# Kernel tuning notes

Measured on AMD Instinct MI355X. Metric: run time of the kernel, lower is better.

Reference implementation:

```python
import jax, jax.numpy as jnp
import numpy as np

NUM_EXPERTS = 8
K = 2
N_EMBD = 1024
HIDDEN = 4 * N_EMBD
BATCH = 2
SEQ = 1024
LB_SCALE = 0.01
NOISY_STD = 1.0
INIT_S = 0.02


def setup_inputs() -> dict:
    key = jax.random.key(0)
    ks = jax.random.split(key, 8)
    D, H, E = N_EMBD, HIDDEN, NUM_EXPERTS
    return {
        "x": jax.random.normal(ks[0], (BATCH, SEQ, D), jnp.float32),
        "noise": jax.random.normal(ks[1], (BATCH, SEQ, E), jnp.float32),  # torch.randn_like(logits)
        "gate_w": jax.random.normal(ks[2], (E, D), jnp.float32) * INIT_S,
        "noise_weight": jnp.zeros((E,), jnp.float32),  # initialized to zeros in the module
        "w1": jax.random.normal(ks[3], (E, H, D), jnp.float32) * INIT_S,
        "b1": jnp.zeros((E, H), jnp.float32),
        "w2": jax.random.normal(ks[4], (E, H, D), jnp.float32) * INIT_S,
        "b2": jnp.zeros((E, H), jnp.float32),
        "wp": jax.random.normal(ks[5], (E, D, H), jnp.float32) * INIT_S,
        "bp": jnp.zeros((E, D), jnp.float32),
    }


def reference(x, noise, gate_w, noise_weight, w1, b1, w2, b2, wp, bp):
    B, S, D = x.shape
    E = gate_w.shape[0]

    # ---- TopKGateParallel ----
    logits = jnp.einsum('bsd,ed->bse', x, gate_w)           # [B,S,E]
    gate_weights = jax.nn.softmax(logits, axis=-1)
    gw_mean = gate_weights.reshape(-1, E).mean(axis=0)       # [E]
    load_balance_loss = jnp.mean((gw_mean - 1.0 / E) ** 2) * LB_SCALE  # mse vs uniform

    logits_noisy = logits + (noise * NOISY_STD) * noise_weight
    top_v, top_i = jax.lax.top_k(logits_noisy, K)            # [B,S,K]
    # scatter top-k logits into a -inf sea, then softmax -> zeros at non-topk slots
    topk_mask = jnp.sum(jax.nn.one_hot(top_i, E, dtype=jnp.float32), axis=-2) > 0  # [B,S,E]
    sparse_logits = jnp.where(topk_mask, logits_noisy, -jnp.inf)
    top_k_gated_weights = jax.nn.softmax(sparse_logits, axis=-1)  # [B,S,E]

    # ---- expert compute + weighted combine (world_size=1: all experts local) ----
    x_flat = x.reshape(B * S, D)                              # [T,D]
    w_flat = top_k_gated_weights.reshape(B * S, E)            # [T,E]
    y = jnp.zeros_like(x_flat)
    for e in range(E):  # fixed small set of experts
        h = x_flat @ w1[e].T + b1[e]                          # [T,H]
        g = x_flat @ w2[e].T + b2[e]                          # [T,H]
        out_e = (h * jax.nn.silu(g)) @ wp[e].T + bp[e]        # [T,D]
        y = y + w_flat[:, e:e + 1] * out_e
    y = y.reshape(B, S, D)
    return y, load_balance_loss
```

## Files before the change

### kernel.cpp

```cpp
#include <hip/hip_runtime.h>

#define TOK 2048
#define DIM 1024
#define HID 4096
#define NE 8
#define KSPLIT 4
#define TMAX 24
#define NCAST 2048

typedef unsigned short u16;
typedef __attribute__((ext_vector_type(8))) short s16x8;
typedef __attribute__((ext_vector_type(4))) float f32x4;

__device__ __forceinline__ u16 f2b(float f) {
  unsigned u = __builtin_bit_cast(unsigned, f);
  unsigned r = (u + 0x7fffu + ((u >> 16) & 1u)) >> 16;
  return (u16)r;
}

__device__ __forceinline__ void gld_lds16(const void* g, void* l) {
  __builtin_amdgcn_global_load_lds((const __attribute__((address_space(1))) void*)g,
                                   (__attribute__((address_space(3))) void*)l, 16, 0, 0);
}

__global__ __launch_bounds__(256) void k_gate(const float* __restrict__ x,
    const float* __restrict__ noise, const float* __restrict__ gw,
    const float* __restrict__ nw, const float* __restrict__ w1,
    const float* __restrict__ w2, const float* __restrict__ wp,
    u16* __restrict__ w1b, u16* __restrict__ w2b, u16* __restrict__ wpb,
    int* __restrict__ tok_e, float* __restrict__ tok_w,
    int* __restrict__ bhist, float* __restrict__ bgw, u16* __restrict__ x16) {
  if (blockIdx.x >= TOK / 4) {
    const int cb = blockIdx.x - TOK / 4;
    const size_t NPT = (size_t)NE * HID * DIM;
    const size_t stride = (size_t)NCAST * 256 * 8;
    for (size_t i = ((size_t)cb * 256 + threadIdx.x) * 8; i < 3 * NPT; i += stride) {
      const float* in; u16* o; size_t j;
      if (i < NPT)          { in = w1; o = w1b; j = i; }
      else if (i < 2 * NPT) { in = w2; o = w2b; j = i - NPT; }
      else                  { in = wp; o = wpb; j = i - 2 * NPT; }
      float4 a = *(const float4*)(in + j);
      float4 b = *(const float4*)(in + j + 4);
      u16 u[8];
      u[0] = f2b(a.x); u[1] = f2b(a.y); u[2] = f2b(a.z); u[3] = f2b(a.w);
      u[4] = f2b(b.x); u[5] = f2b(b.y); u[6] = f2b(b.z); u[7] = f2b(b.w);
      *(s16x8*)(o + j) = *(const s16x8*)u;
    }
    return;
  }
  const int wid = threadIdx.x >> 6, lane = threadIdx.x & 63;
  const int t = blockIdx.x * 4 + wid;
  const float* xr = x + (size_t)t * DIM + lane * 16;
  float acc[NE];
#pragma unroll
  for (int e = 0; e < NE; ++e) acc[e] = 0.f;
  u16 xb[16];
#pragma unroll
  for (int j = 0; j < 4; ++j) {
    float4 xv = *(const float4*)(xr + j * 4);
    xb[j * 4 + 0] = f2b(xv.x); xb[j * 4 + 1] = f2b(xv.y);
    xb[j * 4 + 2] = f2b(xv.z); xb[j * 4 + 3] = f2b(xv.w);
#pragma unroll
    for (int e = 0; e < NE; ++e) {
      float4 gv = *(const float4*)(gw + e * DIM + lane * 16 + j * 4);
      acc[e] += xv.x * gv.x + xv.y * gv.y + xv.z * gv.z + xv.w * gv.w;
    }
  }
  *(s16x8*)(x16 + (size_t)t * DIM + lane * 16) = *(const s16x8*)xb;
  *(s16x8*)(x16 + (size_t)t * DIM + lane * 16 + 8) = *(const s16x8*)(xb + 8);
#pragma unroll
  for (int e = 0; e < NE; ++e) {
#pragma unroll
    for (int off = 32; off >= 1; off >>= 1) acc[e] += __shfl_xor(acc[e], off);
  }
  float m = acc[0];
#pragma unroll
  for (int e = 1; e < NE; ++e) m = fmaxf(m, acc[e]);
  float p[NE]; float s = 0.f;
#pragma unroll
  for (int e = 0; e < NE; ++e) { p[e] = expf(acc[e] - m); s += p[e]; }
  float inv = 1.f / s;
  float v[NE];
#pragma unroll
  for (int e = 0; e < NE; ++e) v[e] = acc[e] + noise[t * NE + e] * nw[e];
  float v0 = -3.4e38f, v1 = -3.4e38f; int i0 = 0, i1 = 0;
#pragma unroll
  for (int e = 0; e < NE; ++e) {
    float ve = v[e];
    if (ve > v0) { v1 = v0; i1 = i0; v0 = ve; i0 = e; }
    else if (ve > v1) { v1 = ve; i1 = e; }
  }
  float e1 = expf(v1 - v0);
  float den = 1.f + e1;
  float w0 = 1.f / den, w1v = e1 / den;

  __shared__ float pl[4][NE];
  __shared__ int el[4][2];
  if (lane == 0) {
#pragma unroll
    for (int e = 0; e < NE; ++e) pl[wid][e] = p[e] * inv;
    el[wid][0] = i0; el[wid][1] = i1;
    tok_e[t * 2] = i0; tok_e[t * 2 + 1] = i1;
    tok_w[t * 2] = w0; tok_w[t * 2 + 1] = w1v;
  }
  __syncthreads();
  if (threadIdx.x < NE) {
    const int e = threadIdx.x;
    float ps = pl[0][e] + pl[1][e] + pl[2][e] + pl[3][e];
    int h = 0;
#pragma unroll
    for (int j = 0; j < 4; ++j) {
      h += (el[j][0] == e);
      h += (el[j][1] == e);
    }
    bgw[blockIdx.x * NE + e] = ps;
    bhist[blockIdx.x * NE + e] = h;
  }
}

__global__ __launch_bounds__(512) void k_scan(const int* __restrict__ bhist,
    const float* __restrict__ bgw, int* __restrict__ blk_off, int* __restrict__ prefix,
    int* __restrict__ counts, int* __restrict__ tile_tab, float* __restrict__ loss_out) {
  const int i = threadIdx.x, lane = i & 63, wv = i >> 6;
  __shared__ int wsum[8];
  __shared__ float wfs[8];
  __shared__ int etot[8];
  __shared__ float fsum[8];
  for (int e = 0; e < NE; ++e) {
    int v = bhist[i * NE + e];
    int sc = v;
#pragma unroll
    for (int off = 1; off < 64; off <<= 1) {
      int u = __shfl_up(sc, off);
      if (lane >= off) sc += u;
    }
    float f = bgw[i * NE + e];
#pragma unroll
    for (int off = 32; off >= 1; off >>= 1) f += __shfl_xor(f, off);
    if (lane == 63) wsum[wv] = sc;
    if (lane == 0) wfs[wv] = f;
    __syncthreads();
    int base = 0;
    for (int w2 = 0; w2 < wv; ++w2) base += wsum[w2];
    blk_off[i * NE + e] = base + sc - v;
    if (i == 0) {
      float tf = 0.f;
      for (int w2 = 0; w2 < 8; ++w2) tf += wfs[w2];
      fsum[e] = tf;
    }
    if (i == 511) etot[e] = base + sc;
    __syncthreads();
  }
  if (i == 0) {
    int sacc = 0;
    float l = 0.f;
    int tt = 0;
#pragma unroll
    for (int e = 0; e < NE; ++e) { prefix[e] = sacc; counts[e] = etot[e]; sacc += etot[e]; }
    for (int e = 0; e < NE; ++e) {
      const int nmt = (etot[e] + 255) >> 8;
      for (int m2 = 0; m2 < nmt; ++m2) tile_tab[tt++] = (e << 16) | m2;
    }
    for (; tt < TMAX; ++tt) tile_tab[tt] = -1;
#pragma unroll
    for (int e = 0; e < NE; ++e) {
      float d = fsum[e] * (1.f / TOK) - 0.125f;
      l += d * d;
    }
    *loss_out = l * (0.01f / NE);
  }
}

__global__ __launch_bounds__(256) void k_build(const int* __restrict__ tok_e,
    const float* __restrict__ tok_w, const int* __restrict__ prefix,
    const int* __restrict__ blk_off, int* __restrict__ ent, float* __restrict__ entw,
    int* __restrict__ inv) {
  const int t = blockIdx.x * 256 + threadIdx.x;
  const int g = t >> 2;
  const int base = (t & 3) * 2;
  int ee[8];
#pragma unroll
  for (int j = 0; j < 8; ++j) ee[j] = tok_e[g * 8 + j];
#pragma unroll
  for (int s = 0; s < 2; ++s) {
    const int e = ee[base + s];
    int rank = 0;
#pragma unroll
    for (int j = 0; j < 8; ++j) rank += (j < base + s) && (ee[j] == e);
    const int idx = prefix[e] + blk_off[g * NE + e] + rank;
    ent[idx] = t * 2 + s;
    entw[idx] = tok_w[t * 2 + s];
    inv[t * 2 + s] = idx;
  }
}

__global__ __launch_bounds__(512) void k_gemm1f(const u16* __restrict__ x16,
    const u16* __restrict__ w1b, const u16* __restrict__ w2b,
    const float* __restrict__ b1, const float* __restrict__ b2,
    const int* __restrict__ ent, const int* __restrict__ counts,
    const int* __restrict__ prefix, const int* __restrict__ tile_tab,
    u16* __restrict__ act) {
  const int tt = tile_tab[blockIdx.y];
  if (tt < 0) return;
  const int e = tt >> 16, mt = tt & 0xffff, nt = blockIdx.x;
  const int cnt = counts[e];
  const int pfx = prefix[e];
  const int tid = threadIdx.x, w = tid >> 6, l = tid & 63;

  __shared__ u16 smem[2][16384];

  const int r0 = tid >> 2;
  const int c = (tid & 3) ^ ((tid >> 3) & 3);
  int g0 = mt * 256 + r0;       if (g0 >= cnt) g0 = cnt - 1;
  int g1 = mt * 256 + 128 + r0; if (g1 >= cnt) g1 = cnt - 1;
  const u16* sa0 = x16 + (size_t)(ent[pfx + g0] >> 1) * DIM + c * 8;
  const u16* sa1 = x16 + (size_t)(ent[pfx + g1] >> 1) * DIM + c * 8;
  const u16* sb1 = w1b + ((size_t)e * HID + nt * 128 + r0) * DIM + c * 8;
  const u16* sb2 = w2b + ((size_t)e * HID + nt * 128 + r0) * DIM + c * 8;
  const int oA0 = tid * 8, oA1 = 4096 + tid * 8;
  const int oB1 = 8192 + tid * 8, oB2 = 12288 + tid * 8;

  const int wr = w >> 1, wc = w & 1;
  const int xs = ((l >> 4) ^ ((l >> 1) & 3)) * 8;
  const int ra = (wr * 64 + (l & 15)) * 32 + xs;
  const int rb = (wc * 64 + (l & 15)) * 32 + xs;

  f32x4 acc1[4][4], acc2[4][4];
#pragma unroll
  for (int m = 0; m < 4; ++m)
#pragma unroll
    for (int n = 0; n < 4; ++n) {
      acc1[m][n] = (f32x4){0.f, 0.f, 0.f, 0.f};
      acc2[m][n] = (f32x4){0.f, 0.f, 0.f, 0.f};
    }

  auto STAGE = [&](int buf, int k0) {
    gld_lds16(sa0 + k0, &smem[buf][oA0]);
    gld_lds16(sa1 + k0, &smem[buf][oA1]);
    gld_lds16(sb1 + k0, &smem[buf][oB1]);
    gld_lds16(sb2 + k0, &smem[buf][oB2]);
  };

  const int NT = DIM / 32;
  STAGE(0, 0);
  STAGE(1, 32);
  asm volatile("s_waitcnt vmcnt(4)" ::: "memory");
  __builtin_amdgcn_s_barrier();
  __builtin_amdgcn_sched_barrier(0);
  int cur = 0;
  for (int kt = 0; kt < NT; ++kt) {
    const u16* S = &smem[cur][0];
    s16x8 af[4];
#pragma unroll
    for (int m = 0; m < 4; ++m) af[m] = *(const s16x8*)(S + ra + m * 512);
#pragma unroll
    for (int n = 0; n < 4; ++n) {
      s16x8 bf1 = *(const s16x8*)(S + 8192 + rb + n * 512);
      s16x8 bf2 = *(const s16x8*)(S + 12288 + rb + n * 512);
#pragma unroll
      for (int m = 0; m < 4; ++m) {
        acc1[m][n] = __builtin_amdgcn_mfma_f32_16x16x32_bf16(af[m], bf1, acc1[m][n], 0, 0, 0);
        acc2[m][n] = __builtin_amdgcn_mfma_f32_16x16x32_bf16(af[m], bf2, acc2[m][n], 0, 0, 0);
      }
    }
    if (kt + 1 < NT) {
      asm volatile("s_waitcnt lgkmcnt(0)" ::: "memory");
      __builtin_amdgcn_sched_barrier(0);
      __builtin_amdgcn_s_barrier();
      if (kt + 2 < NT) {
        STAGE(cur, (kt + 2) * 32);
        asm volatile("s_waitcnt vmcnt(4)" ::: "memory");
      } else {
        asm volatile("s_waitcnt vmcnt(0)" ::: "memory");
      }
      __builtin_amdgcn_s_barrier();
      __builtin_amdgcn_sched_barrier(0);
    }
    cur ^= 1;
  }

#pragma unroll
  for (int n = 0; n < 4; ++n) {
    const int col = nt * 128 + wc * 64 + n * 16 + (l & 15);
    const float bb1 = b1[(size_t)e * HID + col];
    const float bb2 = b2[(size_t)e * HID + col];
#pragma unroll
    for (int m = 0; m < 4; ++m) {
#pragma unroll
      for (int r = 0; r < 4; ++r) {
        const int row = mt * 256 + wr * 64 + m * 16 + (l >> 4) * 4 + r;
        if (row < cnt) {
          float h = acc1[m][n][r] + bb1;
          float g = acc2[m][n][r] + bb2;
          float a = h * g / (1.f + expf(-g));
          act[(size_t)(pfx + row) * HID + col] = f2b(a);
        }
      }
    }
  }
}

__global__ __launch_bounds__(512) void k_gemm2f(const u16* __restrict__ act,
    const u16* __restrict__ wpb, const float* __restrict__ bp,
    const float* __restrict__ entw, const int* __restrict__ counts,
    const int* __restrict__ prefix, const int* __restrict__ tile_tab,
    float* __restrict__ yp) {
  const int tt = tile_tab[blockIdx.y];
  if (tt < 0) return;
  const int e = tt >> 16, mt = tt & 0xffff;
  const int sk = blockIdx.z, nt = blockIdx.x;
  const int cnt = counts[e];
  const int pfx = prefix[e];
  const int tid = threadIdx.x, w = tid >> 6, l = tid & 63;

  __shared__ u16 smem[2][16384];

  const int r0 = tid >> 2;
  const int c = (tid & 3) ^ ((tid >> 3) & 3);
  int g0 = mt * 256 + r0;       if (g0 >= cnt) g0 = cnt - 1;
  int g1 = mt * 256 + 128 + r0; if (g1 >= cnt) g1 = cnt - 1;
  const int kbase = sk * (HID / KSPLIT);
  const u16* sa0 = act + (size_t)(pfx + g0) * HID + kbase + c * 8;
  const u16* sa1 = act + (size_t)(pfx + g1) * HID + kbase + c * 8;
  const u16* sb0 = wpb + ((size_t)e * DIM + nt * 256 + r0) * HID + kbase + c * 8;
  const u16* sb1 = sb0 + (size_t)128 * HID;
  const int oA0 = tid * 8, oA1 = 4096 + tid * 8;
  const int oB0 = 8192 + tid * 8, oB1 = 12288 + tid * 8;

  const int wr = w >> 2, wc = w & 3;
  const int xs = ((l >> 4) ^ ((l >> 1) & 3)) * 8;
  const int ra = (wr * 128 + (l & 15)) * 32 + xs;
  const int rb = 8192 + (wc * 64 + (l & 15)) * 32 + xs;

  f32x4 acc[8][4];
#pragma unroll
  for (int m = 0; m < 8; ++m)
#pragma unroll
    for (int n = 0; n < 4; ++n) acc[m][n] = (f32x4){0.f, 0.f, 0.f, 0.f};

  auto STAGE = [&](int buf, int k0) {
    gld_lds16(sa0 + k0, &smem[buf][oA0]);
    gld_lds16(sa1 + k0, &smem[buf][oA1]);
    gld_lds16(sb0 + k0, &smem[buf][oB0]);
    gld_lds16(sb1 + k0, &smem[buf][oB1]);
  };

  const int NIT = HID / KSPLIT / 32;
  STAGE(0, 0);
  STAGE(1, 32);
  asm volatile("s_waitcnt vmcnt(4)" ::: "memory");
  __builtin_amdgcn_s_barrier();
  __builtin_amdgcn_sched_barrier(0);
  int cur = 0;
  for (int kt = 0; kt < NIT; ++kt) {
    const u16* S = &smem[cur][0];
#pragma unroll
    for (int n = 0; n < 4; ++n) {
      s16x8 bf = *(const s16x8*)(S + rb + n * 512);
#pragma unroll
      for (int m = 0; m < 8; ++m) {
        s16x8 af = *(const s16x8*)(S + ra + m * 512);
        acc[m][n] = __builtin_amdgcn_mfma_f32_16x16x32_bf16(af, bf, acc[m][n], 0, 0, 0);
      }
    }
    if (kt + 1 < NIT) {
      asm volatile("s_waitcnt lgkmcnt(0)" ::: "memory");
      __builtin_amdgcn_sched_barrier(0);
      __builtin_amdgcn_s_barrier();
      if (kt + 2 < NIT) {
        STAGE(cur, (kt + 2) * 32);
        asm volatile("s_waitcnt vmcnt(4)" ::: "memory");
      } else {
        asm volatile("s_waitcnt vmcnt(0)" ::: "memory");
      }
      __builtin_amdgcn_s_barrier();
      __builtin_amdgcn_sched_barrier(0);
    }
    cur ^= 1;
  }

#pragma unroll
  for (int n = 0; n < 4; ++n) {
    const int col = nt * 256 + wc * 64 + n * 16 + (l & 15);
    const float bpv = (sk == 0) ? bp[(size_t)e * DIM + col] : 0.f;
#pragma unroll
    for (int m = 0; m < 8; ++m) {
#pragma unroll
      for (int r = 0; r < 4; ++r) {
        const int row = mt * 256 + wr * 128 + m * 16 + (l >> 4) * 4 + r;
        if (row < cnt) {
          const int idx = pfx + row;
          yp[((size_t)sk * (TOK * 2) + idx) * DIM + col] = entw[idx] * (acc[m][n][r] + bpv);
        }
      }
    }
  }
}

__global__ __launch_bounds__(256) void k_final(const float* __restrict__ yp,
    const int* __restrict__ inv, float* __restrict__ out) {
  const int t = blockIdx.x;
  const int d = threadIdx.x * 4;
  const int i0 = inv[t * 2], i1 = inv[t * 2 + 1];
  float4 s = {0.f, 0.f, 0.f, 0.f};
#pragma unroll
  for (int sk = 0; sk < KSPLIT; ++sk) {
    float4 a = *(const float4*)(yp + ((size_t)sk * (TOK * 2) + i0) * DIM + d);
    float4 b = *(const float4*)(yp + ((size_t)sk * (TOK * 2) + i1) * DIM + d);
    s.x += a.x + b.x; s.y += a.y + b.y; s.z += a.z + b.z; s.w += a.w + b.w;
  }
  *(float4*)(out + (size_t)t * DIM + d) = s;
}

extern "C" void kernel_launch(void* const* d_in, const int* in_sizes, int n_in,
                              void* d_out, int out_size, void* d_ws, size_t ws_size,
                              hipStream_t stream) {
  const float* x      = (const float*)d_in[0];
  const float* noise  = (const float*)d_in[1];
  const float* gate_w = (const float*)d_in[2];
  const float* nw     = (const float*)d_in[3];
  const float* w1     = (const float*)d_in[4];
  const float* b1     = (const float*)d_in[5];
  const float* w2     = (const float*)d_in[6];
  const float* b2     = (const float*)d_in[7];
  const float* wp     = (const float*)d_in[8];
  const float* bp     = (const float*)d_in[9];
  float* out = (float*)d_out;
  char* ws = (char*)d_ws;

  const size_t SZ_X16 = (size_t)TOK * DIM * 2;
  const size_t SZ_ACT = (size_t)TOK * 2 * HID * 2;
  const size_t SZ_W   = (size_t)NE * HID * DIM * 2;

  u16* x16 = (u16*)ws;
  u16* act = (u16*)(ws + SZ_X16);
  u16* w1b = (u16*)(ws + SZ_X16 + SZ_ACT);
  u16* w2b = (u16*)(ws + SZ_X16 + SZ_ACT + SZ_W);
  u16* wpb = (u16*)(ws + SZ_X16 + SZ_ACT + 2 * SZ_W);
  float* yp = (float*)w1b;
  char* meta = ws + SZ_X16 + SZ_ACT + 3 * SZ_W;
  int*   tok_e    = (int*)(meta);
  float* tok_w    = (float*)(meta + 16384);
  int*   ent      = (int*)(meta + 32768);
  float* entw     = (float*)(meta + 49152);
  int*   bhist    = (int*)(meta + 65536);
  float* bgw      = (float*)(meta + 81920);
  int*   blk_off  = (int*)(meta + 98304);
  int*   inv      = (int*)(meta + 114688);
  int*   counts   = (int*)(meta + 131072);
  int*   prefix   = (int*)(meta + 131072 + 64);
  int*   tile_tab = (int*)(meta + 131072 + 128);

  k_gate<<<TOK / 4 + NCAST, 256, 0, stream>>>(x, noise, gate_w, nw, w1, w2, wp,
                                              w1b, w2b, wpb, tok_e, tok_w, bhist, bgw, x16);
  k_scan<<<1, 512, 0, stream>>>(bhist, bgw, blk_off, prefix, counts, tile_tab,
                                out + (size_t)TOK * DIM);
  k_build<<<TOK / 256, 256, 0, stream>>>(tok_e, tok_w, prefix, blk_off, ent, entw, inv);
  k_gemm1f<<<dim3(HID / 128, TMAX), 512, 0, stream>>>(x16, w1b, w2b, b1, b2, ent,
                                                      counts, prefix, tile_tab, act);
  k_gemm2f<<<dim3(DIM / 256, TMAX, KSPLIT), 512, 0, stream>>>(act, wpb, bp, entw,
                                                              counts, prefix, tile_tab, yp);
  k_final<<<TOK, 256, 0, stream>>>(yp, inv, out);
}
```

Before: 387.6 us.

## Fuse fp32-to-bf16 weight cast into expert GEMM tile loading

```diff
diff --git a/kernel.cpp b/kernel.cpp
--- a/kernel.cpp
+++ b/kernel.cpp
@@ -6,7 +6,6 @@
 #define NE 8
 #define KSPLIT 4
 #define TMAX 24
-#define NCAST 2048
 
 typedef unsigned short u16;
 typedef __attribute__((ext_vector_type(8))) short s16x8;
@@ -25,29 +24,9 @@
 
 __global__ __launch_bounds__(256) void k_gate(const float* __restrict__ x,
     const float* __restrict__ noise, const float* __restrict__ gw,
-    const float* __restrict__ nw, const float* __restrict__ w1,
-    const float* __restrict__ w2, const float* __restrict__ wp,
-    u16* __restrict__ w1b, u16* __restrict__ w2b, u16* __restrict__ wpb,
+    const float* __restrict__ nw,
     int* __restrict__ tok_e, float* __restrict__ tok_w,
     int* __restrict__ bhist, float* __restrict__ bgw, u16* __restrict__ x16) {
-  if (blockIdx.x >= TOK / 4) {
-    const int cb = blockIdx.x - TOK / 4;
-    const size_t NPT = (size_t)NE * HID * DIM;
-    const size_t stride = (size_t)NCAST * 256 * 8;
-    for (size_t i = ((size_t)cb * 256 + threadIdx.x) * 8; i < 3 * NPT; i += stride) {
-      const float* in; u16* o; size_t j;
-      if (i < NPT)          { in = w1; o = w1b; j = i; }
-      else if (i < 2 * NPT) { in = w2; o = w2b; j = i - NPT; }
-      else                  { in = wp; o = wpb; j = i - 2 * NPT; }
-      float4 a = *(const float4*)(in + j);
-      float4 b = *(const float4*)(in + j + 4);
-      u16 u[8];
-      u[0] = f2b(a.x); u[1] = f2b(a.y); u[2] = f2b(a.z); u[3] = f2b(a.w);
-      u[4] = f2b(b.x); u[5] = f2b(b.y); u[6] = f2b(b.z); u[7] = f2b(b.w);
-      *(s16x8*)(o + j) = *(const s16x8*)u;
-    }
-    return;
-  }
   const int wid = threadIdx.x >> 6, lane = threadIdx.x & 63;
   const int t = blockIdx.x * 4 + wid;
   const float* xr = x + (size_t)t * DIM + lane * 16;
@@ -195,7 +174,7 @@
 }
 
 __global__ __launch_bounds__(512) void k_gemm1f(const u16* __restrict__ x16,
-    const u16* __restrict__ w1b, const u16* __restrict__ w2b,
+    const float* __restrict__ w1, const float* __restrict__ w2,
     const float* __restrict__ b1, const float* __restrict__ b2,
     const int* __restrict__ ent, const int* __restrict__ counts,
     const int* __restrict__ prefix, const int* __restrict__ tile_tab,
@@ -215,8 +194,8 @@
   int g1 = mt * 256 + 128 + r0; if (g1 >= cnt) g1 = cnt - 1;
   const u16* sa0 = x16 + (size_t)(ent[pfx + g0] >> 1) * DIM + c * 8;
   const u16* sa1 = x16 + (size_t)(ent[pfx + g1] >> 1) * DIM + c * 8;
-  const u16* sb1 = w1b + ((size_t)e * HID + nt * 128 + r0) * DIM + c * 8;
-  const u16* sb2 = w2b + ((size_t)e * HID + nt * 128 + r0) * DIM + c * 8;
+  const float* pB1 = w1 + ((size_t)e * HID + nt * 128 + r0) * DIM + c * 8;
+  const float* pB2 = w2 + ((size_t)e * HID + nt * 128 + r0) * DIM + c * 8;
   const int oA0 = tid * 8, oA1 = 4096 + tid * 8;
   const int oB1 = 8192 + tid * 8, oB2 = 12288 + tid * 8;
 
@@ -234,21 +213,38 @@
       acc2[m][n] = (f32x4){0.f, 0.f, 0.f, 0.f};
     }
 
-  auto STAGE = [&](int buf, int k0) {
+  f32x4 rb0_, rb1_, rb2_, rb3_;
+  auto LOADB = [&](int k0) {
+    rb0_ = *(const f32x4*)(pB1 + k0);
+    rb1_ = *(const f32x4*)(pB1 + k0 + 4);
+    rb2_ = *(const f32x4*)(pB2 + k0);
+    rb3_ = *(const f32x4*)(pB2 + k0 + 4);
+  };
+  auto STAGEA = [&](int buf, int k0) {
     gld_lds16(sa0 + k0, &smem[buf][oA0]);
     gld_lds16(sa1 + k0, &smem[buf][oA1]);
-    gld_lds16(sb1 + k0, &smem[buf][oB1]);
-    gld_lds16(sb2 + k0, &smem[buf][oB2]);
+  };
+  auto WRITEB = [&](int buf) {
+    u16 u[16];
+    u[0] = f2b(rb0_[0]); u[1] = f2b(rb0_[1]); u[2] = f2b(rb0_[2]); u[3] = f2b(rb0_[3]);
+    u[4] = f2b(rb1_[0]); u[5] = f2b(rb1_[1]); u[6] = f2b(rb1_[2]); u[7] = f2b(rb1_[3]);
+    u[8] = f2b(rb2_[0]); u[9] = f2b(rb2_[1]); u[10] = f2b(rb2_[2]); u[11] = f2b(rb2_[3]);
+    u[12] = f2b(rb3_[0]); u[13] = f2b(rb3_[1]); u[14] = f2b(rb3_[2]); u[15] = f2b(rb3_[3]);
+    *(s16x8*)&smem[buf][oB1] = *(const s16x8*)u;
+    *(s16x8*)&smem[buf][oB2] = *(const s16x8*)(u + 8);
   };
 
   const int NT = DIM / 32;
-  STAGE(0, 0);
-  STAGE(1, 32);
-  asm volatile("s_waitcnt vmcnt(4)" ::: "memory");
+  LOADB(0);
+  STAGEA(0, 0);
+  asm volatile("s_waitcnt vmcnt(0)" ::: "memory");
+  WRITEB(0);
+  asm volatile("s_waitcnt lgkmcnt(0)" ::: "memory");
+  __builtin_amdgcn_sched_barrier(0);
   __builtin_amdgcn_s_barrier();
-  __builtin_amdgcn_sched_barrier(0);
   int cur = 0;
   for (int kt = 0; kt < NT; ++kt) {
+    if (kt + 1 < NT) { LOADB((kt + 1) * 32); STAGEA(cur ^ 1, (kt + 1) * 32); }
     const u16* S = &smem[cur][0];
     s16x8 af[4];
 #pragma unroll
@@ -264,17 +260,12 @@
       }
     }
     if (kt + 1 < NT) {
+      asm volatile("s_waitcnt vmcnt(0)" ::: "memory");
+      __builtin_amdgcn_sched_barrier(0);
+      WRITEB(cur ^ 1);
       asm volatile("s_waitcnt lgkmcnt(0)" ::: "memory");
       __builtin_amdgcn_sched_barrier(0);
       __builtin_amdgcn_s_barrier();
-      if (kt + 2 < NT) {
-        STAGE(cur, (kt + 2) * 32);
-        asm volatile("s_waitcnt vmcnt(4)" ::: "memory");
-      } else {
-        asm volatile("s_waitcnt vmcnt(0)" ::: "memory");
-      }
-      __builtin_amdgcn_s_barrier();
-      __builtin_amdgcn_sched_barrier(0);
     }
     cur ^= 1;
   }
@@ -301,7 +292,7 @@
 }
 
 __global__ __launch_bounds__(512) void k_gemm2f(const u16* __restrict__ act,
-    const u16* __restrict__ wpb, const float* __restrict__ bp,
+    const float* __restrict__ wp, const float* __restrict__ bp,
     const float* __restrict__ entw, const int* __restrict__ counts,
     const int* __restrict__ prefix, const int* __restrict__ tile_tab,
     float* __restrict__ yp) {
@@ -322,8 +313,8 @@
   const int kbase = sk * (HID / KSPLIT);
   const u16* sa0 = act + (size_t)(pfx + g0) * HID + kbase + c * 8;
   const u16* sa1 = act + (size_t)(pfx + g1) * HID + kbase + c * 8;
-  const u16* sb0 = wpb + ((size_t)e * DIM + nt * 256 + r0) * HID + kbase + c * 8;
-  const u16* sb1 = sb0 + (size_t)128 * HID;
+  const float* pB0 = wp + ((size_t)e * DIM + nt * 256 + r0) * HID + kbase + c * 8;
+  const float* pB1h = pB0 + (size_t)128 * HID;
   const int oA0 = tid * 8, oA1 = 4096 + tid * 8;
   const int oB0 = 8192 + tid * 8, oB1 = 12288 + tid * 8;
 
@@ -338,21 +329,38 @@
 #pragma unroll
     for (int n = 0; n < 4; ++n) acc[m][n] = (f32x4){0.f, 0.f, 0.f, 0.f};
 
-  auto STAGE = [&](int buf, int k0) {
+  f32x4 rb0_, rb1_, rb2_, rb3_;
+  auto LOADB = [&](int k0) {
+    rb0_ = *(const f32x4*)(pB0 + k0);
+    rb1_ = *(const f32x4*)(pB0 + k0 + 4);
+    rb2_ = *(const f32x4*)(pB1h + k0);
+    rb3_ = *(const f32x4*)(pB1h + k0 + 4);
+  };
+  auto STAGEA = [&](int buf, int k0) {
     gld_lds16(sa0 + k0, &smem[buf][oA0]);
     gld_lds16(sa1 + k0, &smem[buf][oA1]);
-    gld_lds16(sb0 + k0, &smem[buf][oB0]);
-    gld_lds16(sb1 + k0, &smem[buf][oB1]);
+  };
+  auto WRITEB = [&](int buf) {
+    u16 u[16];
+    u[0] = f2b(rb0_[0]); u[1] = f2b(rb0_[1]); u[2] = f2b(rb0_[2]); u[3] = f2b(rb0_[3]);
+    u[4] = f2b(rb1_[0]); u[5] = f2b(rb1_[1]); u[6] = f2b(rb1_[2]); u[7] = f2b(rb1_[3]);
+    u[8] = f2b(rb2_[0]); u[9] = f2b(rb2_[1]); u[10] = f2b(rb2_[2]); u[11] = f2b(rb2_[3]);
+    u[12] = f2b(rb3_[0]); u[13] = f2b(rb3_[1]); u[14] = f2b(rb3_[2]); u[15] = f2b(rb3_[3]);
+    *(s16x8*)&smem[buf][oB0] = *(const s16x8*)u;
+    *(s16x8*)&smem[buf][oB1] = *(const s16x8*)(u + 8);
   };
 
   const int NIT = HID / KSPLIT / 32;
-  STAGE(0, 0);
-  STAGE(1, 32);
-  asm volatile("s_waitcnt vmcnt(4)" ::: "memory");
+  LOADB(0);
+  STAGEA(0, 0);
+  asm volatile("s_waitcnt vmcnt(0)" ::: "memory");
+  WRITEB(0);
+  asm volatile("s_waitcnt lgkmcnt(0)" ::: "memory");
+  __builtin_amdgcn_sched_barrier(0);
   __builtin_amdgcn_s_barrier();
-  __builtin_amdgcn_sched_barrier(0);
   int cur = 0;
   for (int kt = 0; kt < NIT; ++kt) {
+    if (kt + 1 < NIT) { LOADB((kt + 1) * 32); STAGEA(cur ^ 1, (kt + 1) * 32); }
     const u16* S = &smem[cur][0];
 #pragma unroll
     for (int n = 0; n < 4; ++n) {
@@ -364,17 +372,12 @@
       }
     }
     if (kt + 1 < NIT) {
+      asm volatile("s_waitcnt vmcnt(0)" ::: "memory");
+      __builtin_amdgcn_sched_barrier(0);
+      WRITEB(cur ^ 1);
       asm volatile("s_waitcnt lgkmcnt(0)" ::: "memory");
       __builtin_amdgcn_sched_barrier(0);
       __builtin_amdgcn_s_barrier();
-      if (kt + 2 < NIT) {
-        STAGE(cur, (kt + 2) * 32);
-        asm volatile("s_waitcnt vmcnt(4)" ::: "memory");
-      } else {
-        asm volatile("s_waitcnt vmcnt(0)" ::: "memory");
-      }
-      __builtin_amdgcn_s_barrier();
-      __builtin_amdgcn_sched_barrier(0);
     }
     cur ^= 1;
   }
@@ -430,15 +433,12 @@
 
   const size_t SZ_X16 = (size_t)TOK * DIM * 2;
   const size_t SZ_ACT = (size_t)TOK * 2 * HID * 2;
-  const size_t SZ_W   = (size_t)NE * HID * DIM * 2;
-
-  u16* x16 = (u16*)ws;
-  u16* act = (u16*)(ws + SZ_X16);
-  u16* w1b = (u16*)(ws + SZ_X16 + SZ_ACT);
-  u16* w2b = (u16*)(ws + SZ_X16 + SZ_ACT + SZ_W);
-  u16* wpb = (u16*)(ws + SZ_X16 + SZ_ACT + 2 * SZ_W);
-  float* yp = (float*)w1b;
-  char* meta = ws + SZ_X16 + SZ_ACT + 3 * SZ_W;
+  const size_t SZ_YP  = (size_t)KSPLIT * TOK * 2 * DIM * 4;
+
+  u16* x16  = (u16*)ws;
+  u16* act  = (u16*)(ws + SZ_X16);
+  float* yp = (float*)(ws + SZ_X16 + SZ_ACT);
+  char* meta = ws + SZ_X16 + SZ_ACT + SZ_YP;
   int*   tok_e    = (int*)(meta);
   float* tok_w    = (float*)(meta + 16384);
   int*   ent      = (int*)(meta + 32768);
@@ -451,14 +451,13 @@
   int*   prefix   = (int*)(meta + 131072 + 64);
   int*   tile_tab = (int*)(meta + 131072 + 128);
 
-  k_gate<<<TOK / 4 + NCAST, 256, 0, stream>>>(x, noise, gate_w, nw, w1, w2, wp,
-                                              w1b, w2b, wpb, tok_e, tok_w, bhist, bgw, x16);
+  k_gate<<<TOK / 4, 256, 0, stream>>>(x, noise, gate_w, nw, tok_e, tok_w, bhist, bgw, x16);
   k_scan<<<1, 512, 0, stream>>>(bhist, bgw, blk_off, prefix, counts, tile_tab,
                                 out + (size_t)TOK * DIM);
   k_build<<<TOK / 256, 256, 0, stream>>>(tok_e, tok_w, prefix, blk_off, ent, entw, inv);
-  k_gemm1f<<<dim3(HID / 128, TMAX), 512, 0, stream>>>(x16, w1b, w2b, b1, b2, ent,
+  k_gemm1f<<<dim3(HID / 128, TMAX), 512, 0, stream>>>(x16, w1, w2, b1, b2, ent,
                                                       counts, prefix, tile_tab, act);
-  k_gemm2f<<<dim3(DIM / 256, TMAX, KSPLIT), 512, 0, stream>>>(act, wpb, bp, entw,
+  k_gemm2f<<<dim3(DIM / 256, TMAX, KSPLIT), 512, 0, stream>>>(act, wp, bp, entw,
                                                               counts, prefix, tile_tab, yp);
   k_final<<<TOK, 256, 0, stream>>>(yp, inv, out);
 }
```

New measurement: 366.6 us. 1.06x faster.
